# Optimization experiments

Measured on AMD Instinct MI355X. Metric: run time of the kernel, lower is better.

## Reference

```python
import jax, jax.numpy as jnp
import numpy as np

B, D, T, H, OUT = 256, 256, 256, 512, 256

def setup_inputs() -> dict:
    key = jax.random.key(0)
    ks = jax.random.split(key, 7)
    s = lambda fan: 1.0 / np.sqrt(fan)
    x = jax.random.normal(ks[0], (B, D, T), dtype=jnp.float32)
    Wx = jax.random.normal(ks[1], (D, H), dtype=jnp.float32) * s(D)
    Wh = jax.random.normal(ks[2], (H, H), dtype=jnp.float32) * s(H)
    b = jnp.zeros((H,), dtype=jnp.float32)
    Wout = jax.random.normal(ks[3], (H, OUT), dtype=jnp.float32) * s(H)
    bout = jnp.zeros((OUT,), dtype=jnp.float32)
    init_state = jnp.zeros((1, H), dtype=jnp.float32)  # non-trainable zeros in keras
    return {"x": x, "Wx": Wx, "Wh": Wh, "b": b, "Wout": Wout, "bout": bout, "init_state": init_state}

def reference(x, Wx, Wh, b, Wout, bout, init_state):
    # x: [B, D, T] (time on last axis, as unstacked in the keras layer)
    batch = x.shape[0]
    h0 = jnp.tile(init_state, (batch, 1))              # [B, H]
    xs = jnp.moveaxis(x, -1, 0)                        # [T, B, D]
    # precompute input projections for all steps (hoisted out of the recurrence)
    xproj = jnp.einsum('tbd,dh->tbh', xs, Wx) + b      # [T, B, H]

    def step(h_prev, xp):
        cur = jnp.tanh(xp + h_prev @ Wh)
        # residual: state_i = cell_out + state_{i-1}; at i=0 h_prev is zeros, so always adding is exact
        new = cur + h_prev
        return new, new

    _, states = jax.lax.scan(step, h0, xproj)          # states: [T, B, H]
    states = jnp.moveaxis(states, 0, 1)                # [B, T, H]
    out = states @ Wout + bout                         # [B, T, OUT]
    return out
```

## Files before the change

kernel.cpp:

```cpp
#include <hip/hip_runtime.h>
#include <cstring>
#include <cstdio>

typedef __attribute__((ext_vector_type(8))) short short8;
typedef __attribute__((ext_vector_type(4))) float f32x4;
typedef __attribute__((ext_vector_type(4))) unsigned u32x4;

__device__ __forceinline__ short f2bf(float f){
  unsigned u; __builtin_memcpy(&u, &f, 4);
  u += 0x7FFFu + ((u >> 16) & 1u);
  return (short)(u >> 16);
}
__device__ __forceinline__ float bf2f(short s){
  unsigned u = ((unsigned)(unsigned short)s) << 16;
  float f; __builtin_memcpy(&f, &u, 4);
  return f;
}
__device__ __forceinline__ void split2(float v, short& hi, short& lo){
  hi = f2bf(v);
  float r = v - bf2f(hi);
  lo = f2bf(r);
}
__device__ __forceinline__ unsigned pack2(float v){
  short hi, lo; split2(v, hi, lo);
  return (((unsigned)(unsigned short)hi) << 16) | (unsigned)(unsigned short)lo;
}
__device__ __forceinline__ float tanh_fast(float x){
  float e = __expf(2.0f * x);
  return 1.0f - 2.0f / (e + 1.0f);
}

#define HIDX(r,k) ((((r) * 512) + (k)) ^ (((r) & 7) << 3))

__global__ void transpose_split(const float* __restrict__ in,
                                short* __restrict__ outh, short* __restrict__ outl,
                                int R, int C){
  int idx = blockIdx.x * 256 + threadIdx.x;
  if (idx < R * C){
    int r = idx / C, c = idx % C;
    short h, l; split2(in[(size_t)r * C + c], h, l);
    outh[(size_t)c * R + r] = h;
    outl[(size_t)c * R + r] = l;
  }
}

__global__ void transpose_to_bf16(const float* __restrict__ in, short* __restrict__ out,
                                  int R, int C){
  int idx = blockIdx.x * 256 + threadIdx.x;
  if (idx < R * C){
    int r = idx / C, c = idx % C;
    out[(size_t)c * R + r] = f2bf(in[(size_t)r * C + c]);
  }
}

__global__ __launch_bounds__(256) void transpose_x_split(const float* __restrict__ x,
                                                         short* __restrict__ xTh,
                                                         short* __restrict__ xTl){
  __shared__ float tile[64][65];
  const int b = blockIdx.x, d0 = blockIdx.y * 64, t0 = blockIdx.z * 64;
  const int tid = threadIdx.x;
  const float* xp = x + ((size_t)b * 256 + d0) * 256 + t0;
  for (int v = tid; v < 1024; v += 256){
    int r = v >> 4, c4 = (v & 15) * 4;
    float4 f = *(const float4*)(xp + (size_t)r * 256 + c4);
    tile[r][c4+0] = f.x; tile[r][c4+1] = f.y; tile[r][c4+2] = f.z; tile[r][c4+3] = f.w;
  }
  __syncthreads();
  for (int v = tid; v < 512; v += 256){
    int j = v >> 3, i8 = (v & 7) * 8;
    short8 oh, ol;
    #pragma unroll
    for (int u = 0; u < 8; ++u){ short h, l; split2(tile[i8 + u][j], h, l); oh[u] = h; ol[u] = l; }
    size_t off = ((size_t)(t0 + j) * 256 + b) * 256 + d0 + i8;
    *(short8*)(xTh + off) = oh;
    *(short8*)(xTl + off) = ol;
  }
}

__global__ __launch_bounds__(256) void gemm1_split(
    const short* __restrict__ Ah, const short* __restrict__ Al,
    const short* __restrict__ Bh, const short* __restrict__ Bl,
    const float* __restrict__ bias, float* __restrict__ C0, float* __restrict__ C1,
    int M, int N, int K)
{
  __shared__ short lAh[128][72];
  __shared__ short lAl[128][72];
  __shared__ short lBh[128][72];
  __shared__ short lBl[128][72];
  const int m0 = blockIdx.y * 128, n0 = blockIdx.x * 128;
  const int tid = threadIdx.x;
  const int lane = tid & 63, wave = tid >> 6;
  const int wm = (wave >> 1) * 64, wn = (wave & 1) * 64;
  f32x4 acc[4][4] = {};
  for (int k0 = 0; k0 < K; k0 += 64){
    __syncthreads();
    for (int v = tid; v < 4096; v += 256){
      int sel = v >> 10, idx = v & 1023;
      int r = idx >> 3, c = (idx & 7) * 8;
      const short* src = (sel == 0) ? Ah + (size_t)(m0 + r) * K + k0 + c
                       : (sel == 1) ? Al + (size_t)(m0 + r) * K + k0 + c
                       : (sel == 2) ? Bh + (size_t)(n0 + r) * K + k0 + c
                                    : Bl + (size_t)(n0 + r) * K + k0 + c;
      short8 val = *(const short8*)src;
      short* dst = (sel == 0) ? &lAh[r][c] : (sel == 1) ? &lAl[r][c]
                 : (sel == 2) ? &lBh[r][c] : &lBl[r][c];
      *(short8*)dst = val;
    }
    __syncthreads();
    #pragma unroll
    for (int kk = 0; kk < 64; kk += 32){
      int ko = kk + (lane >> 4) * 8;
      short8 ah[4], al[4], bh[4], bl[4];
      #pragma unroll
      for (int i = 0; i < 4; ++i){
        ah[i] = *(const short8*)&lAh[wm + i * 16 + (lane & 15)][ko];
        al[i] = *(const short8*)&lAl[wm + i * 16 + (lane & 15)][ko];
        bh[i] = *(const short8*)&lBh[wn + i * 16 + (lane & 15)][ko];
        bl[i] = *(const short8*)&lBl[wn + i * 16 + (lane & 15)][ko];
      }
      #pragma unroll
      for (int i = 0; i < 4; ++i)
      #pragma unroll
      for (int j = 0; j < 4; ++j){
        acc[i][j] = __builtin_amdgcn_mfma_f32_16x16x32_bf16(ah[i], bh[j], acc[i][j], 0, 0, 0);
        acc[i][j] = __builtin_amdgcn_mfma_f32_16x16x32_bf16(ah[i], bl[j], acc[i][j], 0, 0, 0);
        acc[i][j] = __builtin_amdgcn_mfma_f32_16x16x32_bf16(al[i], bh[j], acc[i][j], 0, 0, 0);
      }
    }
  }
  const int cr = (lane >> 4) * 4, cc = lane & 15;
  #pragma unroll
  for (int i = 0; i < 4; ++i)
  #pragma unroll
  for (int j = 0; j < 4; ++j){
    int row = m0 + wm + i * 16 + cr;
    int col = n0 + wn + j * 16 + cc;
    float bv = bias[col];
    float* base = (row < 32768) ? C0 : C1;
    int rr = (row < 32768) ? row : row - 32768;
    #pragma unroll
    for (int r = 0; r < 4; ++r){
      base[(size_t)(rr + r) * N + col] = acc[i][j][r] + bv;
    }
  }
}

__global__ __launch_bounds__(256, 1) void rnn_steps_v9(
    const float* __restrict__ xp0,
    const float* __restrict__ xp1,
    const short* __restrict__ WhTh,
    const short* __restrict__ WhTl,
    const float* __restrict__ init,
    short* __restrict__ states,
    unsigned* __restrict__ pay,
    unsigned* __restrict__ flags)
{
  __shared__ short hh[16 * 512];
  __shared__ short hl[16 * 512];
  const int tid = threadIdx.x, lane = tid & 63, wave = tid >> 6;
  const int team = blockIdx.x & 31, slice = blockIdx.x >> 5;
  const int b0 = team * 8;
  const int nc = slice * 64 + wave * 16;

  short8 Bh[16], Bl[16];
  {
    const size_t col = (size_t)(nc + (lane & 15));
    const int kb0 = (lane >> 4) * 8;
    #pragma unroll
    for (int ks = 0; ks < 16; ++ks){
      Bh[ks] = *(const short8*)(WhTh + col * 512 + ks * 32 + kb0);
      Bl[ks] = *(const short8*)(WhTl + col * 512 + ks * 32 + kb0);
    }
    #pragma unroll
    for (int ks = 0; ks < 16; ++ks){
      asm volatile("" : "+v"(Bh[ks]), "+v"(Bl[ks]));
    }
  }
  for (int v = tid; v < 8 * 512; v += 256){
    int r = 8 + (v >> 9), k = v & 511;
    hh[HIDX(r, k)] = 0; hl[HIDX(r, k)] = 0;
  }
  for (int v = tid; v < 8 * 512; v += 256){
    int r = v >> 9, k = v & 511;
    short hi, lo; split2(init[k], hi, lo);
    hh[HIDX(r, k)] = hi; hl[HIDX(r, k)] = lo;
  }
  __syncthreads();

  const int cc = lane & 15;
  const bool islo = (lane < 32);
  const int mbase = ((lane & 31) >> 4) * 4;
  const int m_0 = mbase + (islo ? 0 : 2);
  const int m_1 = mbase + (islo ? 1 : 3);
  const int n = nc + cc;
  float hr0 = init[n], hr1 = init[n];

  const int am = lane & 15, kb = (lane >> 4) * 8;
  const int rr = tid & 7, c0 = ((tid >> 3) & 31) * 16;

  u32x4 pf0 = {}, pf1 = {};

  for (int t = 0; t < 256; ++t){
    float xv0, xv1;
    if (t == 0){
      xv0 = xp0[(size_t)(b0 + m_0) * 512 + n];
      xv1 = xp0[(size_t)(b0 + m_1) * 512 + n];
    } else {
      const unsigned tagv = (unsigned)t;
      bool ok = (pf0.x >= tagv || slice == 0) && (pf0.y >= tagv || slice == 1) &&
                (pf0.z >= tagv || slice == 2) && (pf0.w >= tagv || slice == 3) &&
                (pf1.x >= tagv || slice == 4) && (pf1.y >= tagv || slice == 5) &&
                (pf1.z >= tagv || slice == 6) && (pf1.w >= tagv || slice == 7);
      if (!ok){
        const unsigned* flg = flags + (((size_t)(t & 1)) * 32 + team) * 32;
        while (true){
          __builtin_amdgcn_s_sleep(1);
          u32x4 f0, f1;
          asm volatile("global_load_dwordx4 %0, %1, off sc0 sc1" : "=&v"(f0) : "v"(flg)     : "memory");
          asm volatile("global_load_dwordx4 %0, %1, off sc0 sc1" : "=&v"(f1) : "v"(flg + 4) : "memory");
          asm volatile("s_waitcnt vmcnt(0)" : "+v"(f0), "+v"(f1) :: "memory");
          bool ok2 = (f0.x >= tagv || slice == 0) && (f0.y >= tagv || slice == 1) &&
                     (f0.z >= tagv || slice == 2) && (f0.w >= tagv || slice == 3) &&
                     (f1.x >= tagv || slice == 4) && (f1.y >= tagv || slice == 5) &&
                     (f1.z >= tagv || slice == 6) && (f1.w >= tagv || slice == 7);
          if (ok2) break;
        }
      }
      const unsigned* src = pay + ((((size_t)(t & 1)) * 32 + team) * 8 + rr) * 512 + c0;
      u32x4 g0, g1, g2, g3;
      asm volatile("global_load_dwordx4 %0, %1, off sc0 sc1" : "=&v"(g0) : "v"(src +  0) : "memory");
      asm volatile("global_load_dwordx4 %0, %1, off sc0 sc1" : "=&v"(g1) : "v"(src +  4) : "memory");
      asm volatile("global_load_dwordx4 %0, %1, off sc0 sc1" : "=&v"(g2) : "v"(src +  8) : "memory");
      asm volatile("global_load_dwordx4 %0, %1, off sc0 sc1" : "=&v"(g3) : "v"(src + 12) : "memory");
      const float* xpb = (t < 128) ? xp0 : xp1;
      const int tt = (t < 128) ? t : t - 128;
      const float* xa0 = xpb + ((size_t)tt * 256 + b0 + m_0) * 512 + n;
      const float* xa1 = xpb + ((size_t)tt * 256 + b0 + m_1) * 512 + n;
      asm volatile("global_load_dword %0, %1, off" : "=&v"(xv0) : "v"(xa0) : "memory");
      asm volatile("global_load_dword %0, %1, off" : "=&v"(xv1) : "v"(xa1) : "memory");
      asm volatile("s_waitcnt vmcnt(2)"
                   : "+v"(g0), "+v"(g1), "+v"(g2), "+v"(g3) :: "memory");
      short8 h0v, h1v, l0v, l1v;
      h0v[0] = (short)(g0.x >> 16); h0v[1] = (short)(g0.y >> 16);
      h0v[2] = (short)(g0.z >> 16); h0v[3] = (short)(g0.w >> 16);
      h0v[4] = (short)(g1.x >> 16); h0v[5] = (short)(g1.y >> 16);
      h0v[6] = (short)(g1.z >> 16); h0v[7] = (short)(g1.w >> 16);
      h1v[0] = (short)(g2.x >> 16); h1v[1] = (short)(g2.y >> 16);
      h1v[2] = (short)(g2.z >> 16); h1v[3] = (short)(g2.w >> 16);
      h1v[4] = (short)(g3.x >> 16); h1v[5] = (short)(g3.y >> 16);
      h1v[6] = (short)(g3.z >> 16); h1v[7] = (short)(g3.w >> 16);
      l0v[0] = (short)(g0.x & 0xffffu); l0v[1] = (short)(g0.y & 0xffffu);
      l0v[2] = (short)(g0.z & 0xffffu); l0v[3] = (short)(g0.w & 0xffffu);
      l0v[4] = (short)(g1.x & 0xffffu); l0v[5] = (short)(g1.y & 0xffffu);
      l0v[6] = (short)(g1.z & 0xffffu); l0v[7] = (short)(g1.w & 0xffffu);
      l1v[0] = (short)(g2.x & 0xffffu); l1v[1] = (short)(g2.y & 0xffffu);
      l1v[2] = (short)(g2.z & 0xffffu); l1v[3] = (short)(g2.w & 0xffffu);
      l1v[4] = (short)(g3.x & 0xffffu); l1v[5] = (short)(g3.y & 0xffffu);
      l1v[6] = (short)(g3.z & 0xffffu); l1v[7] = (short)(g3.w & 0xffffu);
      *(short8*)&hh[HIDX(rr, c0)]     = h0v;
      *(short8*)&hh[HIDX(rr, c0 + 8)] = h1v;
      *(short8*)&hl[HIDX(rr, c0)]     = l0v;
      *(short8*)&hl[HIDX(rr, c0 + 8)] = l1v;
      __syncthreads();
    }

    f32x4 ahh = {}, ahl = {}, alh = {};
    #pragma unroll
    for (int ks = 0; ks < 16; ++ks){
      short8 Ah = *(const short8*)&hh[HIDX(am, ks * 32 + kb)];
      short8 Al = *(const short8*)&hl[HIDX(am, ks * 32 + kb)];
      ahh = __builtin_amdgcn_mfma_f32_16x16x32_bf16(Ah, Bh[ks], ahh, 0, 0, 0);
      ahl = __builtin_amdgcn_mfma_f32_16x16x32_bf16(Ah, Bl[ks], ahl, 0, 0, 0);
      alh = __builtin_amdgcn_mfma_f32_16x16x32_bf16(Al, Bh[ks], alh, 0, 0, 0);
    }
    const float s0 = ahh[0] + (ahl[0] + alh[0]);
    const float s1 = ahh[1] + (ahl[1] + alh[1]);
    const float s2 = ahh[2] + (ahl[2] + alh[2]);
    const float s3 = ahh[3] + (ahl[3] + alh[3]);
    const float t2 = __shfl(s2, lane ^ 32);
    const float t3 = __shfl(s3, lane ^ 32);
    const float v0 = islo ? s0 : t2;
    const float v1 = islo ? s1 : t3;

    if (t > 0){
      asm volatile("s_waitcnt vmcnt(0)" : "+v"(xv0), "+v"(xv1) :: "memory");
    }
    const float hn0 = tanh_fast(xv0 + v0) + hr0;
    const float hn1 = tanh_fast(xv1 + v1) + hr1;
    hr0 = hn0; hr1 = hn1;

    if (t < 255){
      unsigned* dst = pay + ((((size_t)((t + 1) & 1)) * 32 + team) * 8) * 512;
      unsigned w0 = pack2(hn0), w1 = pack2(hn1);
      unsigned* a0 = dst + (size_t)m_0 * 512 + n;
      unsigned* a1 = dst + (size_t)m_1 * 512 + n;
      asm volatile("global_store_dword %0, %1, off sc0 sc1" :: "v"(a0), "v"(w0) : "memory");
      asm volatile("global_store_dword %0, %1, off sc0 sc1" :: "v"(a1), "v"(w1) : "memory");
      states[((size_t)(b0 + m_0) * 256 + t) * 512 + n] = f2bf(hn0);
      states[((size_t)(b0 + m_1) * 256 + t) * 512 + n] = f2bf(hn1);
      const unsigned* nflg = flags + (((size_t)((t + 1) & 1)) * 32 + team) * 32;
      asm volatile("global_load_dwordx4 %0, %1, off sc0 sc1" : "=&v"(pf0) : "v"(nflg)     : "memory");
      asm volatile("global_load_dwordx4 %0, %1, off sc0 sc1" : "=&v"(pf1) : "v"(nflg + 4) : "memory");
      asm volatile("s_waitcnt vmcnt(0)" : "+v"(pf0), "+v"(pf1) :: "memory");
      __syncthreads();
      if (tid == 0){
        unsigned* fdst = flags + (((size_t)((t + 1) & 1)) * 32 + team) * 32 + slice;
        unsigned tagn = (unsigned)(t + 1);
        asm volatile("global_store_dword %0, %1, off sc0 sc1" :: "v"(fdst), "v"(tagn) : "memory");
      }
    } else {
      states[((size_t)(b0 + m_0) * 256 + t) * 512 + n] = f2bf(hn0);
      states[((size_t)(b0 + m_1) * 256 + t) * 512 + n] = f2bf(hn1);
    }
  }
}

__global__ __launch_bounds__(256) void gemm_bias_f32(
    const short* __restrict__ A, const short* __restrict__ Bt,
    const float* __restrict__ bias, float* __restrict__ C,
    int M, int N, int K)
{
  __shared__ short lA[128][72];
  __shared__ short lB[128][72];
  const int m0 = blockIdx.y * 128, n0 = blockIdx.x * 128;
  const int tid = threadIdx.x;
  const int lane = tid & 63, wave = tid >> 6;
  const int wm = (wave >> 1) * 64, wn = (wave & 1) * 64;
  f32x4 acc[4][4] = {};
  for (int k0 = 0; k0 < K; k0 += 64){
    __syncthreads();
    for (int v = tid; v < 2048; v += 256){
      int sel = v >> 10, idx = v & 1023;
      int r = idx >> 3, c = (idx & 7) * 8;
      const short* src = (sel == 0) ? A + (size_t)(m0 + r) * K + k0 + c
                                    : Bt + (size_t)(n0 + r) * K + k0 + c;
      short8 val = *(const short8*)src;
      short* dst = (sel == 0) ? &lA[r][c] : &lB[r][c];
      *(short8*)dst = val;
    }
    __syncthreads();
    #pragma unroll
    for (int kk = 0; kk < 64; kk += 32){
      int ko = kk + (lane >> 4) * 8;
      short8 a[4], b[4];
      #pragma unroll
      for (int i = 0; i < 4; ++i){
        a[i] = *(const short8*)&lA[wm + i * 16 + (lane & 15)][ko];
        b[i] = *(const short8*)&lB[wn + i * 16 + (lane & 15)][ko];
      }
      #pragma unroll
      for (int i = 0; i < 4; ++i)
      #pragma unroll
      for (int j = 0; j < 4; ++j){
        acc[i][j] = __builtin_amdgcn_mfma_f32_16x16x32_bf16(a[i], b[j], acc[i][j], 0, 0, 0);
      }
    }
  }
  const int cr = (lane >> 4) * 4, cc = lane & 15;
  #pragma unroll
  for (int i = 0; i < 4; ++i)
  #pragma unroll
  for (int j = 0; j < 4; ++j){
    int row = m0 + wm + i * 16 + cr;
    int col = n0 + wn + j * 16 + cc;
    float bv = bias[col];
    #pragma unroll
    for (int r = 0; r < 4; ++r){
      C[(size_t)(row + r) * N + col] = acc[i][j][r] + bv;
    }
  }
}

extern "C" void kernel_launch(void* const* d_in, const int* in_sizes, int n_in,
                              void* d_out, int out_size, void* d_ws, size_t ws_size,
                              hipStream_t stream){
  (void)in_sizes; (void)n_in; (void)out_size;
  const float* x    = (const float*)d_in[0];
  const float* Wx   = (const float*)d_in[1];
  const float* Wh   = (const float*)d_in[2];
  const float* bias = (const float*)d_in[3];
  const float* Wout = (const float*)d_in[4];
  const float* bout = (const float*)d_in[5];
  const float* init = (const float*)d_in[6];
  float* out = (float*)d_out;

  char* p = (char*)d_ws;
  short* xTh    = (short*)(p);
  short* xTl    = (short*)(p + 33554432);
  short* states = (short*)(p);
  float* xproj0 = (float*)(p + 67108864);
  float* xproj1 = (float*)d_out;
  short* WxTh   = (short*)(p + 134217728);
  short* WxTl   = (short*)(p + 134479872);
  short* WhTh   = (short*)(p + 134742016);
  short* WhTl   = (short*)(p + 135266304);
  short* WoutT  = (short*)(p + 135790592);
  unsigned* pay   = (unsigned*)(p + 136052736);
  unsigned* flags = (unsigned*)(p + 137101312);
  if (ws_size < 137109504u){
    fprintf(stderr, "kernel_launch: ws_size=%zu < 137109504 needed\n", ws_size);
  }

  hipMemsetAsync(flags, 0, 8192, stream);

  transpose_split<<<(256*512 + 255)/256, 256, 0, stream>>>(Wx, WxTh, WxTl, 256, 512);
  transpose_split<<<(512*512 + 255)/256, 256, 0, stream>>>(Wh, WhTh, WhTl, 512, 512);
  transpose_to_bf16<<<(512*256 + 255)/256, 256, 0, stream>>>(Wout, WoutT, 512, 256);
  transpose_x_split<<<dim3(256, 4, 4), 256, 0, stream>>>(x, xTh, xTl);
  gemm1_split<<<dim3(4, 512), 256, 0, stream>>>(xTh, xTl, WxTh, WxTl, bias,
                                                xproj0, xproj1, 65536, 512, 256);
  rnn_steps_v9<<<256, 256, 0, stream>>>(xproj0, xproj1, WhTh, WhTl, init,
                                        states, pay, flags);
  gemm_bias_f32<<<dim3(2, 512), 256, 0, stream>>>(states, WoutT, bout, out, 65536, 256, 512);
}
```

Before: 977.9 us.

## Tag recurrent state payloads and double-buffer LDS to cut per-step sync

Each hidden-state word written to global memory now carries its step number in the upper 32 bits. Consumers poll the payload until every tag matches, so correctness no longer depends on the flag write ordering. The LDS h buffers are double-buffered, which removes the trailing __syncthreads before the flag store. The state writes and xproj loads are also moved off the critical poll path. In exchange, payload traffic doubles, the flag spin is still kept, and there is extra polling on the payload itself.

```diff
diff --git a/kernel.cpp b/kernel.cpp
--- a/kernel.cpp
+++ b/kernel.cpp
@@ -145,18 +145,18 @@
   }
 }
 
-__global__ __launch_bounds__(256, 1) void rnn_steps_v9(
+__global__ __launch_bounds__(256, 1) void rnn_steps_v12(
     const float* __restrict__ xp0,
     const float* __restrict__ xp1,
     const short* __restrict__ WhTh,
     const short* __restrict__ WhTl,
     const float* __restrict__ init,
     short* __restrict__ states,
-    unsigned* __restrict__ pay,
+    unsigned long long* __restrict__ pay,
     unsigned* __restrict__ flags)
 {
-  __shared__ short hh[16 * 512];
-  __shared__ short hl[16 * 512];
+  __shared__ short hh[2 * 16 * 512];
+  __shared__ short hl[2 * 16 * 512];
   const int tid = threadIdx.x, lane = tid & 63, wave = tid >> 6;
   const int team = blockIdx.x & 31, slice = blockIdx.x >> 5;
   const int b0 = team * 8;
@@ -178,12 +178,15 @@
   }
   for (int v = tid; v < 8 * 512; v += 256){
     int r = 8 + (v >> 9), k = v & 511;
-    hh[HIDX(r, k)] = 0; hl[HIDX(r, k)] = 0;
+    int ix = HIDX(r, k);
+    hh[ix] = 0; hh[8192 + ix] = 0;
+    hl[ix] = 0; hl[8192 + ix] = 0;
   }
   for (int v = tid; v < 8 * 512; v += 256){
     int r = v >> 9, k = v & 511;
     short hi, lo; split2(init[k], hi, lo);
-    hh[HIDX(r, k)] = hi; hl[HIDX(r, k)] = lo;
+    int ix = HIDX(r, k);
+    hh[ix] = hi; hl[ix] = lo;
   }
   __syncthreads();
 
@@ -196,79 +199,79 @@
   float hr0 = init[n], hr1 = init[n];
 
   const int am = lane & 15, kb = (lane >> 4) * 8;
-  const int rr = tid & 7, c0 = ((tid >> 3) & 31) * 16;
-
-  u32x4 pf0 = {}, pf1 = {};
+  const int rr = tid >> 5, c0 = (tid & 31) * 16;
 
   for (int t = 0; t < 256; ++t){
-    float xv0, xv1;
-    if (t == 0){
-      xv0 = xp0[(size_t)(b0 + m_0) * 512 + n];
-      xv1 = xp0[(size_t)(b0 + m_1) * 512 + n];
-    } else {
+    const float* xpb = (t < 128) ? xp0 : xp1;
+    const int tt = (t < 128) ? t : t - 128;
+    const float xv0 = xpb[((size_t)tt * 256 + b0 + m_0) * 512 + n];
+    const float xv1 = xpb[((size_t)tt * 256 + b0 + m_1) * 512 + n];
+    const int buf = (t & 1) * 8192;
+
+    if (t > 0){
       const unsigned tagv = (unsigned)t;
-      bool ok = (pf0.x >= tagv || slice == 0) && (pf0.y >= tagv || slice == 1) &&
-                (pf0.z >= tagv || slice == 2) && (pf0.w >= tagv || slice == 3) &&
-                (pf1.x >= tagv || slice == 4) && (pf1.y >= tagv || slice == 5) &&
-                (pf1.z >= tagv || slice == 6) && (pf1.w >= tagv || slice == 7);
-      if (!ok){
-        const unsigned* flg = flags + (((size_t)(t & 1)) * 32 + team) * 32;
-        while (true){
-          __builtin_amdgcn_s_sleep(1);
-          u32x4 f0, f1;
-          asm volatile("global_load_dwordx4 %0, %1, off sc0 sc1" : "=&v"(f0) : "v"(flg)     : "memory");
-          asm volatile("global_load_dwordx4 %0, %1, off sc0 sc1" : "=&v"(f1) : "v"(flg + 4) : "memory");
-          asm volatile("s_waitcnt vmcnt(0)" : "+v"(f0), "+v"(f1) :: "memory");
-          bool ok2 = (f0.x >= tagv || slice == 0) && (f0.y >= tagv || slice == 1) &&
-                     (f0.z >= tagv || slice == 2) && (f0.w >= tagv || slice == 3) &&
-                     (f1.x >= tagv || slice == 4) && (f1.y >= tagv || slice == 5) &&
-                     (f1.z >= tagv || slice == 6) && (f1.w >= tagv || slice == 7);
-          if (ok2) break;
-        }
-      }
-      const unsigned* src = pay + ((((size_t)(t & 1)) * 32 + team) * 8 + rr) * 512 + c0;
-      u32x4 g0, g1, g2, g3;
-      asm volatile("global_load_dwordx4 %0, %1, off sc0 sc1" : "=&v"(g0) : "v"(src +  0) : "memory");
-      asm volatile("global_load_dwordx4 %0, %1, off sc0 sc1" : "=&v"(g1) : "v"(src +  4) : "memory");
-      asm volatile("global_load_dwordx4 %0, %1, off sc0 sc1" : "=&v"(g2) : "v"(src +  8) : "memory");
-      asm volatile("global_load_dwordx4 %0, %1, off sc0 sc1" : "=&v"(g3) : "v"(src + 12) : "memory");
-      const float* xpb = (t < 128) ? xp0 : xp1;
-      const int tt = (t < 128) ? t : t - 128;
-      const float* xa0 = xpb + ((size_t)tt * 256 + b0 + m_0) * 512 + n;
-      const float* xa1 = xpb + ((size_t)tt * 256 + b0 + m_1) * 512 + n;
-      asm volatile("global_load_dword %0, %1, off" : "=&v"(xv0) : "v"(xa0) : "memory");
-      asm volatile("global_load_dword %0, %1, off" : "=&v"(xv1) : "v"(xa1) : "memory");
-      asm volatile("s_waitcnt vmcnt(2)"
-                   : "+v"(g0), "+v"(g1), "+v"(g2), "+v"(g3) :: "memory");
+      const unsigned* flg = flags + (((size_t)(t & 1)) * 32 + team) * 32;
+      while (true){
+        u32x4 f0, f1;
+        asm volatile("global_load_dwordx4 %0, %1, off sc0 sc1" : "=&v"(f0) : "v"(flg)     : "memory");
+        asm volatile("global_load_dwordx4 %0, %1, off sc0 sc1" : "=&v"(f1) : "v"(flg + 4) : "memory");
+        asm volatile("s_waitcnt vmcnt(0)" : "+v"(f0), "+v"(f1) :: "memory");
+        if (f0.x >= tagv && f0.y >= tagv && f0.z >= tagv && f0.w >= tagv &&
+            f1.x >= tagv && f1.y >= tagv && f1.z >= tagv && f1.w >= tagv) break;
+        __builtin_amdgcn_s_sleep(1);
+      }
+      const unsigned long long* src =
+          pay + ((((size_t)(t & 1)) * 32 + team) * 8 + rr) * 512 + c0;
+      u32x4 g[8];
+      bool need0 = true, need1 = true, need2 = true, need3 = true;
+      bool need4 = true, need5 = true, need6 = true, need7 = true;
+      while (true){
+        if (need0) asm volatile("global_load_dwordx4 %0, %1, off sc0 sc1" : "=&v"(g[0]) : "v"(src +  0) : "memory");
+        if (need1) asm volatile("global_load_dwordx4 %0, %1, off sc0 sc1" : "=&v"(g[1]) : "v"(src +  2) : "memory");
+        if (need2) asm volatile("global_load_dwordx4 %0, %1, off sc0 sc1" : "=&v"(g[2]) : "v"(src +  4) : "memory");
+        if (need3) asm volatile("global_load_dwordx4 %0, %1, off sc0 sc1" : "=&v"(g[3]) : "v"(src +  6) : "memory");
+        if (need4) asm volatile("global_load_dwordx4 %0, %1, off sc0 sc1" : "=&v"(g[4]) : "v"(src +  8) : "memory");
+        if (need5) asm volatile("global_load_dwordx4 %0, %1, off sc0 sc1" : "=&v"(g[5]) : "v"(src + 10) : "memory");
+        if (need6) asm volatile("global_load_dwordx4 %0, %1, off sc0 sc1" : "=&v"(g[6]) : "v"(src + 12) : "memory");
+        if (need7) asm volatile("global_load_dwordx4 %0, %1, off sc0 sc1" : "=&v"(g[7]) : "v"(src + 14) : "memory");
+        asm volatile("s_waitcnt vmcnt(0)"
+                     : "+v"(g[0]), "+v"(g[1]), "+v"(g[2]), "+v"(g[3]),
+                       "+v"(g[4]), "+v"(g[5]), "+v"(g[6]), "+v"(g[7]) :: "memory");
+        need0 = (g[0].y != tagv) | (g[0].w != tagv);
+        need1 = (g[1].y != tagv) | (g[1].w != tagv);
+        need2 = (g[2].y != tagv) | (g[2].w != tagv);
+        need3 = (g[3].y != tagv) | (g[3].w != tagv);
+        need4 = (g[4].y != tagv) | (g[4].w != tagv);
+        need5 = (g[5].y != tagv) | (g[5].w != tagv);
+        need6 = (g[6].y != tagv) | (g[6].w != tagv);
+        need7 = (g[7].y != tagv) | (g[7].w != tagv);
+        if (!(need0 | need1 | need2 | need3 | need4 | need5 | need6 | need7)) break;
+        __builtin_amdgcn_s_sleep(1);
+      }
       short8 h0v, h1v, l0v, l1v;
-      h0v[0] = (short)(g0.x >> 16); h0v[1] = (short)(g0.y >> 16);
-      h0v[2] = (short)(g0.z >> 16); h0v[3] = (short)(g0.w >> 16);
-      h0v[4] = (short)(g1.x >> 16); h0v[5] = (short)(g1.y >> 16);
-      h0v[6] = (short)(g1.z >> 16); h0v[7] = (short)(g1.w >> 16);
-      h1v[0] = (short)(g2.x >> 16); h1v[1] = (short)(g2.y >> 16);
-      h1v[2] = (short)(g2.z >> 16); h1v[3] = (short)(g2.w >> 16);
-      h1v[4] = (short)(g3.x >> 16); h1v[5] = (short)(g3.y >> 16);
-      h1v[6] = (short)(g3.z >> 16); h1v[7] = (short)(g3.w >> 16);
-      l0v[0] = (short)(g0.x & 0xffffu); l0v[1] = (short)(g0.y & 0xffffu);
-      l0v[2] = (short)(g0.z & 0xffffu); l0v[3] = (short)(g0.w & 0xffffu);
-      l0v[4] = (short)(g1.x & 0xffffu); l0v[5] = (short)(g1.y & 0xffffu);
-      l0v[6] = (short)(g1.z & 0xffffu); l0v[7] = (short)(g1.w & 0xffffu);
-      l1v[0] = (short)(g2.x & 0xffffu); l1v[1] = (short)(g2.y & 0xffffu);
-      l1v[2] = (short)(g2.z & 0xffffu); l1v[3] = (short)(g2.w & 0xffffu);
-      l1v[4] = (short)(g3.x & 0xffffu); l1v[5] = (short)(g3.y & 0xffffu);
-      l1v[6] = (short)(g3.z & 0xffffu); l1v[7] = (short)(g3.w & 0xffffu);
-      *(short8*)&hh[HIDX(rr, c0)]     = h0v;
-      *(short8*)&hh[HIDX(rr, c0 + 8)] = h1v;
-      *(short8*)&hl[HIDX(rr, c0)]     = l0v;
-      *(short8*)&hl[HIDX(rr, c0 + 8)] = l1v;
-      __syncthreads();
+      #pragma unroll
+      for (int i = 0; i < 4; ++i){
+        unsigned pa = g[i].x,     pb = g[i].z;
+        unsigned pc = g[4 + i].x, pd = g[4 + i].z;
+        h0v[2*i]   = (short)(pa >> 16); h0v[2*i+1] = (short)(pb >> 16);
+        l0v[2*i]   = (short)(pa & 0xffffu); l0v[2*i+1] = (short)(pb & 0xffffu);
+        h1v[2*i]   = (short)(pc >> 16); h1v[2*i+1] = (short)(pd >> 16);
+        l1v[2*i]   = (short)(pc & 0xffffu); l1v[2*i+1] = (short)(pd & 0xffffu);
+      }
+      *(short8*)&hh[buf + HIDX(rr, c0)]     = h0v;
+      *(short8*)&hh[buf + HIDX(rr, c0 + 8)] = h1v;
+      *(short8*)&hl[buf + HIDX(rr, c0)]     = l0v;
+      *(short8*)&hl[buf + HIDX(rr, c0 + 8)] = l1v;
+      asm volatile("s_waitcnt lgkmcnt(0)" ::: "memory");
+      __builtin_amdgcn_s_barrier();
+      __builtin_amdgcn_sched_barrier(0);
     }
 
     f32x4 ahh = {}, ahl = {}, alh = {};
     #pragma unroll
     for (int ks = 0; ks < 16; ++ks){
-      short8 Ah = *(const short8*)&hh[HIDX(am, ks * 32 + kb)];
-      short8 Al = *(const short8*)&hl[HIDX(am, ks * 32 + kb)];
+      short8 Ah = *(const short8*)&hh[buf + HIDX(am, ks * 32 + kb)];
+      short8 Al = *(const short8*)&hl[buf + HIDX(am, ks * 32 + kb)];
       ahh = __builtin_amdgcn_mfma_f32_16x16x32_bf16(Ah, Bh[ks], ahh, 0, 0, 0);
       ahl = __builtin_amdgcn_mfma_f32_16x16x32_bf16(Ah, Bl[ks], ahl, 0, 0, 0);
       alh = __builtin_amdgcn_mfma_f32_16x16x32_bf16(Al, Bh[ks], alh, 0, 0, 0);
@@ -282,36 +285,28 @@
     const float v0 = islo ? s0 : t2;
     const float v1 = islo ? s1 : t3;
 
-    if (t > 0){
-      asm volatile("s_waitcnt vmcnt(0)" : "+v"(xv0), "+v"(xv1) :: "memory");
-    }
     const float hn0 = tanh_fast(xv0 + v0) + hr0;
     const float hn1 = tanh_fast(xv1 + v1) + hr1;
     hr0 = hn0; hr1 = hn1;
 
     if (t < 255){
-      unsigned* dst = pay + ((((size_t)((t + 1) & 1)) * 32 + team) * 8) * 512;
-      unsigned w0 = pack2(hn0), w1 = pack2(hn1);
-      unsigned* a0 = dst + (size_t)m_0 * 512 + n;
-      unsigned* a1 = dst + (size_t)m_1 * 512 + n;
-      asm volatile("global_store_dword %0, %1, off sc0 sc1" :: "v"(a0), "v"(w0) : "memory");
-      asm volatile("global_store_dword %0, %1, off sc0 sc1" :: "v"(a1), "v"(w1) : "memory");
-      states[((size_t)(b0 + m_0) * 256 + t) * 512 + n] = f2bf(hn0);
-      states[((size_t)(b0 + m_1) * 256 + t) * 512 + n] = f2bf(hn1);
-      const unsigned* nflg = flags + (((size_t)((t + 1) & 1)) * 32 + team) * 32;
-      asm volatile("global_load_dwordx4 %0, %1, off sc0 sc1" : "=&v"(pf0) : "v"(nflg)     : "memory");
-      asm volatile("global_load_dwordx4 %0, %1, off sc0 sc1" : "=&v"(pf1) : "v"(nflg + 4) : "memory");
-      asm volatile("s_waitcnt vmcnt(0)" : "+v"(pf0), "+v"(pf1) :: "memory");
-      __syncthreads();
+      const unsigned tagn = (unsigned)(t + 1);
+      unsigned long long* dst =
+          pay + ((((size_t)((t + 1) & 1)) * 32 + team) * 8) * 512;
+      unsigned long long w0 = (((unsigned long long)tagn) << 32) | pack2(hn0);
+      unsigned long long w1 = (((unsigned long long)tagn) << 32) | pack2(hn1);
+      unsigned long long* a0 = dst + (size_t)m_0 * 512 + n;
+      unsigned long long* a1 = dst + (size_t)m_1 * 512 + n;
+      asm volatile("global_store_dwordx2 %0, %1, off sc0 sc1" :: "v"(a0), "v"(w0) : "memory");
+      asm volatile("global_store_dwordx2 %0, %1, off sc0 sc1" :: "v"(a1), "v"(w1) : "memory");
+      __builtin_amdgcn_s_barrier();
       if (tid == 0){
         unsigned* fdst = flags + (((size_t)((t + 1) & 1)) * 32 + team) * 32 + slice;
-        unsigned tagn = (unsigned)(t + 1);
         asm volatile("global_store_dword %0, %1, off sc0 sc1" :: "v"(fdst), "v"(tagn) : "memory");
       }
-    } else {
-      states[((size_t)(b0 + m_0) * 256 + t) * 512 + n] = f2bf(hn0);
-      states[((size_t)(b0 + m_1) * 256 + t) * 512 + n] = f2bf(hn1);
-    }
+    }
+    states[((size_t)(b0 + m_0) * 256 + t) * 512 + n] = f2bf(hn0);
+    states[((size_t)(b0 + m_1) * 256 + t) * 512 + n] = f2bf(hn1);
   }
 }
 
@@ -395,13 +390,13 @@
   short* WhTh   = (short*)(p + 134742016);
   short* WhTl   = (short*)(p + 135266304);
   short* WoutT  = (short*)(p + 135790592);
-  unsigned* pay   = (unsigned*)(p + 136052736);
-  unsigned* flags = (unsigned*)(p + 137101312);
-  if (ws_size < 137109504u){
-    fprintf(stderr, "kernel_launch: ws_size=%zu < 137109504 needed\n", ws_size);
-  }
-
-  hipMemsetAsync(flags, 0, 8192, stream);
+  unsigned long long* pay = (unsigned long long*)(p + 136052736);
+  unsigned* flags = (unsigned*)(p + 138149888);
+  if (ws_size < 138158080u){
+    fprintf(stderr, "kernel_launch: ws_size=%zu < 138158080 needed\n", ws_size);
+  }
+
+  hipMemsetAsync(pay, 0, 2105344, stream);
 
   transpose_split<<<(256*512 + 255)/256, 256, 0, stream>>>(Wx, WxTh, WxTl, 256, 512);
   transpose_split<<<(512*512 + 255)/256, 256, 0, stream>>>(Wh, WhTh, WhTl, 512, 512);
@@ -409,7 +404,7 @@
   transpose_x_split<<<dim3(256, 4, 4), 256, 0, stream>>>(x, xTh, xTl);
   gemm1_split<<<dim3(4, 512), 256, 0, stream>>>(xTh, xTl, WxTh, WxTl, bias,
                                                 xproj0, xproj1, 65536, 512, 256);
-  rnn_steps_v9<<<256, 256, 0, stream>>>(xproj0, xproj1, WhTh, WhTl, init,
-                                        states, pay, flags);
+  rnn_steps_v12<<<256, 256, 0, stream>>>(xproj0, xproj1, WhTh, WhTl, init,
+                                         states, pay, flags);
   gemm_bias_f32<<<dim3(2, 512), 256, 0, stream>>>(states, WoutT, bout, out, 65536, 256, 512);
 }
```

Result: slower. 1.327 ms (+35.7%).
